# Kernel optimization log

Measured on AMD Instinct MI355X. Metric: run time of the kernel, lower is better.

The kernel has to match this reference:

```python
import jax, jax.numpy as jnp
import numpy as np

H = 32  # num_heads
ROPE_BASE = 10000.0


def _rope(x, offset):
    # x: [B, H, S, D]; rotate-half RoPE with position offset
    B, h, S, D = x.shape
    pos = offset + jnp.arange(S, dtype=jnp.float32)              # [S]
    inv_freq = 1.0 / (ROPE_BASE ** (jnp.arange(0, D, 2, dtype=jnp.float32) / D))  # [D/2]
    ang = pos[:, None] * inv_freq[None, :]                        # [S, D/2]
    cos = jnp.concatenate([jnp.cos(ang), jnp.cos(ang)], axis=-1)  # [S, D]
    sin = jnp.concatenate([jnp.sin(ang), jnp.sin(ang)], axis=-1)  # [S, D]
    x1, x2 = x[..., : D // 2], x[..., D // 2 :]
    rot = jnp.concatenate([-x2, x1], axis=-1)
    return x * cos + rot * sin


def setup_inputs() -> dict:
    key = jax.random.key(0)
    ks = jax.random.split(key, 8)
    B, S, HD = 8, 16, 4096
    Dh = HD // H
    PAST = 4080
    inp = {
        "x": jax.random.normal(ks[0], (B, S, HD), dtype=jnp.float32),
        "past_key": jax.random.normal(ks[1], (B, H, PAST, Dh), dtype=jnp.float32),
        "past_value": jax.random.normal(ks[2], (B, H, PAST, Dh), dtype=jnp.float32),
        "Wq": jax.random.normal(ks[3], (HD, HD), dtype=jnp.float32) * 0.02,
        "bq": jnp.zeros((HD,), dtype=jnp.float32),
        "Wk": jax.random.normal(ks[4], (HD, HD), dtype=jnp.float32) * 0.02,
        "bk": jnp.zeros((HD,), dtype=jnp.float32),
        "Wv": jax.random.normal(ks[5], (HD, HD), dtype=jnp.float32) * 0.02,
        "bv": jnp.zeros((HD,), dtype=jnp.float32),
        "Wo": jax.random.normal(ks[6], (HD, HD), dtype=jnp.float32) * 0.02,
        "bo": jnp.zeros((HD,), dtype=jnp.float32),
    }
    return inp


def reference(x, past_key, past_value, Wq, bq, Wk, bk, Wv, bv, Wo, bo):
    B, S, HD = x.shape
    Dh = HD // H
    scale = Dh ** -0.5
    past_len = past_key.shape[2]

    def split_heads(t):  # [B,S,HD] -> [B,H,S,Dh]
        return t.reshape(B, S, H, Dh).transpose(0, 2, 1, 3)

    Q = split_heads(x @ Wq.T + bq)
    K = split_heads(x @ Wk.T + bk)
    V = split_heads(x @ Wv.T + bv)

    Q = _rope(Q, past_len)
    K = _rope(K, past_len)

    K = jnp.concatenate([past_key, K], axis=2)   # [B,H,past+S,Dh]
    V = jnp.concatenate([past_value, V], axis=2)

    scores = jnp.einsum("bhqd,bhkd->bhqk", Q, K) * scale
    attn = jax.nn.softmax(scores, axis=-1)       # dropout: identity in eval
    out = jnp.einsum("bhqk,bhkd->bhqd", attn, V)
    out = out.transpose(0, 2, 1, 3).reshape(B, S, HD)
    out = out @ Wo.T + bo
    return out, attn, (K, V)
```

## Files before the change

### kernel.cpp

```cpp
#include <hip/hip_runtime.h>
#include <hip/hip_bf16.h>

#define BB 8
#define SS 16
#define HH 32
#define DH 128
#define HD 4096
#define PAST 4080
#define TOT 4096
#define MM 128

#define OUT_O  0
#define ATTN_O 524288
#define K_O    17301504
#define V_O    151519232

#define QR_O 0
#define OH_O 524288
#define RT_O 1048576
#define PW_O 1050624

typedef __attribute__((ext_vector_type(8))) short short8;
typedef __attribute__((ext_vector_type(4))) float f32x4;

static __device__ inline unsigned short f2bf(float x) {
  __hip_bfloat16 h = __float2bfloat16(x);
  return *reinterpret_cast<unsigned short*>(&h);
}

__global__ void rope_table_kernel(float* __restrict__ rt) {
  int t = threadIdx.x;
  int s = t >> 6, j = t & 63;
  double inv = exp(-((double)(2 * j) / 128.0) * log(10000.0));
  double ang = (double)(PAST + s) * inv;
  rt[t] = (float)cos(ang);
  rt[1024 + t] = (float)sin(ang);
}

#define LDP 72
__global__ __launch_bounds__(256) void gemm_mfma(
    const float* __restrict__ A, const float* __restrict__ W0,
    const float* __restrict__ W1, const float* __restrict__ W2,
    float* __restrict__ P) {
  int bx = blockIdx.x;
  int mat = bx >> 8;
  int rem = bx & 255;
  int nc = rem >> 3, ks = rem & 7;
  const float* Wm = (mat == 0) ? W0 : ((mat == 1) ? W1 : W2);
  int n0 = nc * 128;
  int tid = threadIdx.x;
  int lane = tid & 63, wid = tid >> 6;
  int wm = wid >> 1, wn = wid & 1;
  int l15 = lane & 15, l4 = lane >> 4;

  __shared__ unsigned short As[128 * LDP];
  __shared__ unsigned short Bs[128 * LDP];

  f32x4 acc[4][4];
#pragma unroll
  for (int i = 0; i < 4; ++i)
#pragma unroll
    for (int j = 0; j < 4; ++j) acc[i][j] = (f32x4){0.f, 0.f, 0.f, 0.f};

  int srow = tid >> 1;
  int skh = (tid & 1) * 32;

  for (int kt = 0; kt < 8; ++kt) {
    int k0 = ks * 512 + kt * 64;
    const float* Ap = &A[(size_t)srow * 4096 + k0 + skh];
    const float* Wp = &Wm[(size_t)(n0 + srow) * 4096 + k0 + skh];
    float4 va[8], vb[8];
#pragma unroll
    for (int i = 0; i < 8; ++i) {
      va[i] = *(const float4*)(Ap + 4 * i);
      vb[i] = *(const float4*)(Wp + 4 * i);
    }
    __syncthreads();
    unsigned short* Asp = &As[srow * LDP + skh];
    unsigned short* Bsp = &Bs[srow * LDP + skh];
#pragma unroll
    for (int i = 0; i < 8; ++i) {
      ushort4 ua, ub;
      ua.x = f2bf(va[i].x); ua.y = f2bf(va[i].y);
      ua.z = f2bf(va[i].z); ua.w = f2bf(va[i].w);
      ub.x = f2bf(vb[i].x); ub.y = f2bf(vb[i].y);
      ub.z = f2bf(vb[i].z); ub.w = f2bf(vb[i].w);
      *(ushort4*)(Asp + 4 * i) = ua;
      *(ushort4*)(Bsp + 4 * i) = ub;
    }
    __syncthreads();
#pragma unroll
    for (int s = 0; s < 2; ++s) {
      short8 af[4], bf[4];
#pragma unroll
      for (int f = 0; f < 4; ++f) {
        int ar = wm * 64 + f * 16 + l15;
        af[f] = *(const short8*)&As[ar * LDP + s * 32 + l4 * 8];
        int br = wn * 64 + f * 16 + l15;
        bf[f] = *(const short8*)&Bs[br * LDP + s * 32 + l4 * 8];
      }
#pragma unroll
      for (int i = 0; i < 4; ++i)
#pragma unroll
        for (int j = 0; j < 4; ++j)
          acc[i][j] = __builtin_amdgcn_mfma_f32_16x16x32_bf16(
              af[i], bf[j], acc[i][j], 0, 0, 0);
    }
  }

  float* Pb = P + (size_t)(mat * 8 + ks) * 524288 + n0;
#pragma unroll
  for (int i = 0; i < 4; ++i) {
#pragma unroll
    for (int j = 0; j < 4; ++j) {
      int mbase = wm * 64 + i * 16 + l4 * 4;
      int nn = wn * 64 + j * 16 + l15;
#pragma unroll
      for (int r = 0; r < 4; ++r)
        Pb[(size_t)(mbase + r) * 4096 + nn] = acc[i][j][r];
    }
  }
}

__global__ __launch_bounds__(256) void qkv_reduce(
    const float* __restrict__ P, const float* __restrict__ bq,
    const float* __restrict__ bk, const float* __restrict__ bv,
    const float* __restrict__ rt, float* __restrict__ qr,
    float* __restrict__ kout, float* __restrict__ vout) {
  int t = blockIdx.x * 256 + threadIdx.x;
  int d2 = t & 63;
  int h = (t >> 6) & 31;
  int m = (t >> 11) & 127;
  int mat = t >> 18;
  int n1 = h * 128 + d2, n2 = n1 + 64;
  const float* bias = (mat == 0) ? bq : ((mat == 1) ? bk : bv);
  float v1 = bias[n1], v2 = bias[n2];
  const float* Pm = P + (size_t)(mat * 8) * 524288 + (size_t)m * 4096;
#pragma unroll
  for (int s = 0; s < 8; ++s) {
    v1 += Pm[(size_t)s * 524288 + n1];
    v2 += Pm[(size_t)s * 524288 + n2];
  }
  int st = m & 15, b = m >> 4;
  int bh = b * 32 + h;
  if (mat == 2) {
    size_t dst = (size_t)(bh * TOT + PAST + st) * 128;
    vout[dst + d2] = v1; vout[dst + 64 + d2] = v2;
  } else {
    float c = rt[st * 64 + d2], sn = rt[1024 + st * 64 + d2];
    float o1 = v1 * c - v2 * sn;
    float o2 = v2 * c + v1 * sn;
    if (mat == 0) {
      size_t dst = (size_t)(bh * 16 + st) * 128;
      qr[dst + d2] = o1; qr[dst + 64 + d2] = o2;
    } else {
      size_t dst = (size_t)(bh * TOT + PAST + st) * 128;
      kout[dst + d2] = o1; kout[dst + 64 + d2] = o2;
    }
  }
}

__global__ __launch_bounds__(256) void scores_kernel(
    const float* __restrict__ pastk, const float* __restrict__ qr,
    float* __restrict__ kout, float* __restrict__ attn) {
  int bh = blockIdx.x >> 5, kc = blockIdx.x & 31;
  int r0 = kc * 128;
  int tid = threadIdx.x;
  __shared__ float KsT[64][129];
  __shared__ float Qs[2048];
#pragma unroll
  for (int i = 0; i < 8; ++i)
    Qs[tid + i * 256] = qr[(size_t)bh * 2048 + tid + i * 256];

  const float4* pk4 = (const float4*)pastk;
  float4* ko4 = (float4*)kout;
  int qg = tid >> 6, lane = tid & 63;
  float acc[4][2] = {{0.f, 0.f}, {0.f, 0.f}, {0.f, 0.f}, {0.f, 0.f}};

  for (int p = 0; p < 2; ++p) {
    if (p) __syncthreads();
#pragma unroll
    for (int i = 0; i < 8; ++i) {
      int f = tid + i * 256;
      int r = f >> 4, g16 = f & 15;
      int g = g16 + p * 16;
      int row = r0 + r;
      float4 v;
      size_t kidx = (size_t)(bh * TOT + row) * 32 + g;
      if (row < PAST) {
        v = pk4[(size_t)(bh * PAST + row) * 32 + g];
        ko4[kidx] = v;
      } else {
        v = ko4[kidx];
      }
      int dl = g16 * 4;
      KsT[dl][r] = v.x; KsT[dl + 1][r] = v.y;
      KsT[dl + 2][r] = v.z; KsT[dl + 3][r] = v.w;
    }
    __syncthreads();
    int dbase = p * 64;
#pragma unroll 4
    for (int d = 0; d < 64; ++d) {
      float k0v = KsT[d][lane], k1v = KsT[d][lane + 64];
#pragma unroll
      for (int j = 0; j < 4; ++j) {
        float qv = Qs[(qg * 4 + j) * 128 + dbase + d];
        acc[j][0] = fmaf(qv, k0v, acc[j][0]);
        acc[j][1] = fmaf(qv, k1v, acc[j][1]);
      }
    }
  }
  const float scale = 0.088388347648318447f;
#pragma unroll
  for (int j = 0; j < 4; ++j) {
    int q = qg * 4 + j;
    size_t base = (size_t)(bh * 16 + q) * 4096 + r0;
    attn[base + lane] = acc[j][0] * scale;
    attn[base + 64 + lane] = acc[j][1] * scale;
  }
}

__global__ __launch_bounds__(256) void softmax_kernel(float* __restrict__ attn) {
  int row = blockIdx.x;
  float4* a4 = (float4*)(attn + (size_t)row * 4096);
  int tid = threadIdx.x;
  float4 v[4];
  float mx = -1e30f;
#pragma unroll
  for (int i = 0; i < 4; ++i) {
    v[i] = a4[tid + i * 256];
    mx = fmaxf(mx, fmaxf(fmaxf(v[i].x, v[i].y), fmaxf(v[i].z, v[i].w)));
  }
#pragma unroll
  for (int off = 32; off; off >>= 1) mx = fmaxf(mx, __shfl_xor(mx, off));
  __shared__ float redm[4];
  __shared__ float reds[4];
  int wid = tid >> 6;
  if ((tid & 63) == 0) redm[wid] = mx;
  __syncthreads();
  mx = fmaxf(fmaxf(redm[0], redm[1]), fmaxf(redm[2], redm[3]));
  float sum = 0.f;
#pragma unroll
  for (int i = 0; i < 4; ++i) {
    v[i].x = __expf(v[i].x - mx); v[i].y = __expf(v[i].y - mx);
    v[i].z = __expf(v[i].z - mx); v[i].w = __expf(v[i].w - mx);
    sum += v[i].x + v[i].y + v[i].z + v[i].w;
  }
#pragma unroll
  for (int off = 32; off; off >>= 1) sum += __shfl_xor(sum, off);
  if ((tid & 63) == 0) reds[wid] = sum;
  __syncthreads();
  sum = reds[0] + reds[1] + reds[2] + reds[3];
  float inv = 1.f / sum;
#pragma unroll
  for (int i = 0; i < 4; ++i) {
    v[i].x *= inv; v[i].y *= inv; v[i].z *= inv; v[i].w *= inv;
    a4[tid + i * 256] = v[i];
  }
}

__global__ __launch_bounds__(256) void pv_kernel(
    const float* __restrict__ pastv, const float* __restrict__ attn,
    float* __restrict__ vout, float* __restrict__ pvp) {
  int blk = blockIdx.x;
  int bh = blk >> 2, nc = blk & 3;
  int tid = threadIdx.x;
  int dq = tid & 31, rg = tid >> 5;
  __shared__ float atn[16][256];
  __shared__ float red[4][16][128];
  float acc[16][4];
#pragma unroll
  for (int q = 0; q < 16; ++q)
#pragma unroll
    for (int j = 0; j < 4; ++j) acc[q][j] = 0.f;

  const float4* pv4 = (const float4*)pastv;
  float4* vo4 = (float4*)vout;
  int base0 = nc * 1024;

  for (int slab = 0; slab < 4; ++slab) {
    int kbase = base0 + slab * 256;
#pragma unroll
    for (int q = 0; q < 16; ++q)
      atn[q][tid] = attn[(size_t)(bh * 16 + q) * 4096 + kbase + tid];
    __syncthreads();
#pragma unroll 4
    for (int it = 0; it < 32; ++it) {
      int kk = it * 8 + rg;
      int row = kbase + kk;
      float4 v;
      size_t oidx = (size_t)(bh * TOT + row) * 32 + dq;
      if (row < PAST) {
        v = pv4[(size_t)(bh * PAST + row) * 32 + dq];
        vo4[oidx] = v;
      } else {
        v = vo4[oidx];
      }
#pragma unroll
      for (int q = 0; q < 16; ++q) {
        float a = atn[q][kk];
        acc[q][0] = fmaf(a, v.x, acc[q][0]);
        acc[q][1] = fmaf(a, v.y, acc[q][1]);
        acc[q][2] = fmaf(a, v.z, acc[q][2]);
        acc[q][3] = fmaf(a, v.w, acc[q][3]);
      }
    }
    __syncthreads();
  }
#pragma unroll
  for (int q = 0; q < 16; ++q)
#pragma unroll
    for (int j = 0; j < 4; ++j) acc[q][j] += __shfl_xor(acc[q][j], 32);
  int wid = tid >> 6;
  if ((tid & 63) < 32) {
#pragma unroll
    for (int q = 0; q < 16; ++q) {
      float4 o; o.x = acc[q][0]; o.y = acc[q][1]; o.z = acc[q][2]; o.w = acc[q][3];
      *(float4*)&red[wid][q][dq * 4] = o;
    }
  }
  __syncthreads();
#pragma unroll
  for (int rep = 0; rep < 8; ++rep) {
    int o = tid + rep * 256;
    int q = o >> 7, dd = o & 127;
    float s = red[0][q][dd] + red[1][q][dd] + red[2][q][dd] + red[3][q][dd];
    pvp[((size_t)(bh * 4 + nc) * 16 + q) * 128 + dd] = s;
  }
}

__global__ __launch_bounds__(256) void pv_reduce(
    const float* __restrict__ pvp, float* __restrict__ oh) {
  int t = blockIdx.x * 256 + threadIdx.x;
  int dd = t & 127;
  int q = (t >> 7) & 15;
  int bh = t >> 11;
  int b = bh >> 5, h = bh & 31;
  float s = 0.f;
#pragma unroll
  for (int nc = 0; nc < 4; ++nc)
    s += pvp[((size_t)(bh * 4 + nc) * 16 + q) * 128 + dd];
  oh[(size_t)(b * 16 + q) * 4096 + h * 128 + dd] = s;
}

__global__ __launch_bounds__(256) void out_reduce(
    const float* __restrict__ P, const float* __restrict__ bo,
    float* __restrict__ out) {
  int t = blockIdx.x * 256 + threadIdx.x;
  float v = bo[t & 4095];
#pragma unroll
  for (int s = 0; s < 8; ++s) v += P[(size_t)s * 524288 + t];
  out[t] = v;
}

extern "C" void kernel_launch(void* const* d_in, const int* in_sizes, int n_in,
                              void* d_out, int out_size, void* d_ws, size_t ws_size,
                              hipStream_t stream) {
  const float* x     = (const float*)d_in[0];
  const float* pastk = (const float*)d_in[1];
  const float* pastv = (const float*)d_in[2];
  const float* Wq = (const float*)d_in[3];
  const float* bq = (const float*)d_in[4];
  const float* Wk = (const float*)d_in[5];
  const float* bk = (const float*)d_in[6];
  const float* Wv = (const float*)d_in[7];
  const float* bv = (const float*)d_in[8];
  const float* Wo = (const float*)d_in[9];
  const float* bo = (const float*)d_in[10];

  float* out  = (float*)d_out;
  float* attn = out + ATTN_O;
  float* kout = out + K_O;
  float* vout = out + V_O;

  float* ws = (float*)d_ws;
  float* qr = ws + QR_O;
  float* oh = ws + OH_O;
  float* rt = ws + RT_O;
  float* pw = ws + PW_O;

  rope_table_kernel<<<1, 1024, 0, stream>>>(rt);
  gemm_mfma<<<768, 256, 0, stream>>>(x, Wq, Wk, Wv, attn);
  qkv_reduce<<<3072, 256, 0, stream>>>(attn, bq, bk, bv, rt, qr, kout, vout);
  scores_kernel<<<8192, 256, 0, stream>>>(pastk, qr, kout, attn);
  softmax_kernel<<<4096, 256, 0, stream>>>(attn);
  pv_kernel<<<1024, 256, 0, stream>>>(pastv, attn, vout, pw);
  pv_reduce<<<2048, 256, 0, stream>>>(pw, oh);
  gemm_mfma<<<256, 256, 0, stream>>>(oh, Wo, Wo, Wo, pw);
  out_reduce<<<2048, 256, 0, stream>>>(pw, bo, out);
}
```

Before: 739.2 us.

## Fuse softmax into scores and PV kernels via per-chunk online statistics

Drops the standalone softmax pass. The scores kernel now emits a per-128-key-chunk max and exp-sum for each row, a tiny kernel merges these into a row max and inverse sum, and the PV kernel normalizes the attention values while loading them, writing the final probabilities back. This removes one full read and write of the 64 MB attention matrix. It also switches the K/V cache copies to nontemporal loads and stores and unrolls the PV loop by two rows. The stats buffer reuses the workspace region of oh, which is only written later, so that is safe.

```diff
diff --git a/kernel.cpp b/kernel.cpp
--- a/kernel.cpp
+++ b/kernel.cpp
@@ -17,11 +17,14 @@
 
 #define QR_O 0
 #define OH_O 524288
+#define STATS_O 524288
+#define ROWS_O  786432
 #define RT_O 1048576
 #define PW_O 1050624
 
 typedef __attribute__((ext_vector_type(8))) short short8;
 typedef __attribute__((ext_vector_type(4))) float f32x4;
+typedef __attribute__((ext_vector_type(4))) float f4v;
 
 static __device__ inline unsigned short f2bf(float x) {
   __hip_bfloat16 h = __float2bfloat16(x);
@@ -162,7 +165,8 @@
 
 __global__ __launch_bounds__(256) void scores_kernel(
     const float* __restrict__ pastk, const float* __restrict__ qr,
-    float* __restrict__ kout, float* __restrict__ attn) {
+    float* __restrict__ kout, float* __restrict__ attn,
+    float* __restrict__ stats) {
   int bh = blockIdx.x >> 5, kc = blockIdx.x & 31;
   int r0 = kc * 128;
   int tid = threadIdx.x;
@@ -172,8 +176,8 @@
   for (int i = 0; i < 8; ++i)
     Qs[tid + i * 256] = qr[(size_t)bh * 2048 + tid + i * 256];
 
-  const float4* pk4 = (const float4*)pastk;
-  float4* ko4 = (float4*)kout;
+  const f4v* pk4 = (const f4v*)pastk;
+  f4v* ko4 = (f4v*)kout;
   int qg = tid >> 6, lane = tid & 63;
   float acc[4][2] = {{0.f, 0.f}, {0.f, 0.f}, {0.f, 0.f}, {0.f, 0.f}};
 
@@ -185,14 +189,12 @@
       int r = f >> 4, g16 = f & 15;
       int g = g16 + p * 16;
       int row = r0 + r;
-      float4 v;
       size_t kidx = (size_t)(bh * TOT + row) * 32 + g;
-      if (row < PAST) {
-        v = pk4[(size_t)(bh * PAST + row) * 32 + g];
-        ko4[kidx] = v;
-      } else {
-        v = ko4[kidx];
-      }
+      const f4v* src = (row < PAST)
+          ? (pk4 + ((size_t)(bh * PAST + row) * 32 + g))
+          : (const f4v*)(ko4 + kidx);
+      f4v v = __builtin_nontemporal_load(src);
+      if (row < PAST) __builtin_nontemporal_store(v, ko4 + kidx);
       int dl = g16 * 4;
       KsT[dl][r] = v.x; KsT[dl + 1][r] = v.y;
       KsT[dl + 2][r] = v.z; KsT[dl + 3][r] = v.w;
@@ -212,97 +214,111 @@
   }
   const float scale = 0.088388347648318447f;
 #pragma unroll
+  for (int j = 0; j < 4; ++j) { acc[j][0] *= scale; acc[j][1] *= scale; }
+#pragma unroll
   for (int j = 0; j < 4; ++j) {
     int q = qg * 4 + j;
     size_t base = (size_t)(bh * 16 + q) * 4096 + r0;
-    attn[base + lane] = acc[j][0] * scale;
-    attn[base + 64 + lane] = acc[j][1] * scale;
-  }
-}
-
-__global__ __launch_bounds__(256) void softmax_kernel(float* __restrict__ attn) {
-  int row = blockIdx.x;
-  float4* a4 = (float4*)(attn + (size_t)row * 4096);
-  int tid = threadIdx.x;
-  float4 v[4];
-  float mx = -1e30f;
-#pragma unroll
-  for (int i = 0; i < 4; ++i) {
-    v[i] = a4[tid + i * 256];
-    mx = fmaxf(mx, fmaxf(fmaxf(v[i].x, v[i].y), fmaxf(v[i].z, v[i].w)));
-  }
-#pragma unroll
-  for (int off = 32; off; off >>= 1) mx = fmaxf(mx, __shfl_xor(mx, off));
-  __shared__ float redm[4];
-  __shared__ float reds[4];
-  int wid = tid >> 6;
-  if ((tid & 63) == 0) redm[wid] = mx;
-  __syncthreads();
-  mx = fmaxf(fmaxf(redm[0], redm[1]), fmaxf(redm[2], redm[3]));
-  float sum = 0.f;
-#pragma unroll
-  for (int i = 0; i < 4; ++i) {
-    v[i].x = __expf(v[i].x - mx); v[i].y = __expf(v[i].y - mx);
-    v[i].z = __expf(v[i].z - mx); v[i].w = __expf(v[i].w - mx);
-    sum += v[i].x + v[i].y + v[i].z + v[i].w;
-  }
-#pragma unroll
-  for (int off = 32; off; off >>= 1) sum += __shfl_xor(sum, off);
-  if ((tid & 63) == 0) reds[wid] = sum;
-  __syncthreads();
-  sum = reds[0] + reds[1] + reds[2] + reds[3];
-  float inv = 1.f / sum;
-#pragma unroll
-  for (int i = 0; i < 4; ++i) {
-    v[i].x *= inv; v[i].y *= inv; v[i].z *= inv; v[i].w *= inv;
-    a4[tid + i * 256] = v[i];
-  }
+    attn[base + lane] = acc[j][0];
+    attn[base + 64 + lane] = acc[j][1];
+  }
+#pragma unroll
+  for (int j = 0; j < 4; ++j) {
+    float m = fmaxf(acc[j][0], acc[j][1]);
+#pragma unroll
+    for (int off = 32; off; off >>= 1) m = fmaxf(m, __shfl_xor(m, off));
+    float e = __expf(acc[j][0] - m) + __expf(acc[j][1] - m);
+#pragma unroll
+    for (int off = 32; off; off >>= 1) e += __shfl_xor(e, off);
+    if (lane == 0) {
+      int q = qg * 4 + j;
+      size_t si = ((size_t)(bh * 16 + q) * 32 + kc) * 2;
+      stats[si] = m; stats[si + 1] = e;
+    }
+  }
+}
+
+__global__ __launch_bounds__(256) void stats_reduce(
+    const float* __restrict__ stats, float* __restrict__ rows) {
+  int r = blockIdx.x * 256 + threadIdx.x;
+  float m = -1e30f;
+#pragma unroll
+  for (int c = 0; c < 32; ++c) m = fmaxf(m, stats[((size_t)r * 32 + c) * 2]);
+  float s = 0.f;
+#pragma unroll
+  for (int c = 0; c < 32; ++c)
+    s += stats[((size_t)r * 32 + c) * 2 + 1] *
+         __expf(stats[((size_t)r * 32 + c) * 2] - m);
+  rows[r * 2] = m;
+  rows[r * 2 + 1] = 1.f / s;
 }
 
 __global__ __launch_bounds__(256) void pv_kernel(
-    const float* __restrict__ pastv, const float* __restrict__ attn,
-    float* __restrict__ vout, float* __restrict__ pvp) {
+    const float* __restrict__ pastv, float* __restrict__ attn,
+    const float* __restrict__ rows, float* __restrict__ vout,
+    float* __restrict__ pvp) {
   int blk = blockIdx.x;
   int bh = blk >> 2, nc = blk & 3;
   int tid = threadIdx.x;
   int dq = tid & 31, rg = tid >> 5;
   __shared__ float atn[16][256];
   __shared__ float red[4][16][128];
+  __shared__ float sm[16], si[16];
+  if (tid < 16) {
+    sm[tid] = rows[(bh * 16 + tid) * 2];
+    si[tid] = rows[(bh * 16 + tid) * 2 + 1];
+  }
   float acc[16][4];
 #pragma unroll
   for (int q = 0; q < 16; ++q)
 #pragma unroll
     for (int j = 0; j < 4; ++j) acc[q][j] = 0.f;
 
-  const float4* pv4 = (const float4*)pastv;
-  float4* vo4 = (float4*)vout;
+  const f4v* pv4 = (const f4v*)pastv;
+  f4v* vo4 = (f4v*)vout;
   int base0 = nc * 1024;
+  __syncthreads();
 
   for (int slab = 0; slab < 4; ++slab) {
     int kbase = base0 + slab * 256;
 #pragma unroll
-    for (int q = 0; q < 16; ++q)
-      atn[q][tid] = attn[(size_t)(bh * 16 + q) * 4096 + kbase + tid];
+    for (int q = 0; q < 16; ++q) {
+      size_t ai = (size_t)(bh * 16 + q) * 4096 + kbase + tid;
+      float x = attn[ai];
+      float p = __expf(x - sm[q]) * si[q];
+      atn[q][tid] = p;
+      __builtin_nontemporal_store(p, &attn[ai]);
+    }
     __syncthreads();
-#pragma unroll 4
-    for (int it = 0; it < 32; ++it) {
-      int kk = it * 8 + rg;
-      int row = kbase + kk;
-      float4 v;
-      size_t oidx = (size_t)(bh * TOT + row) * 32 + dq;
-      if (row < PAST) {
-        v = pv4[(size_t)(bh * PAST + row) * 32 + dq];
-        vo4[oidx] = v;
-      } else {
-        v = vo4[oidx];
+#pragma unroll 2
+    for (int it = 0; it < 32; it += 2) {
+      int kk0 = it * 8 + rg, kk1 = kk0 + 8;
+      int row0 = kbase + kk0, row1 = kbase + kk1;
+      size_t o0 = (size_t)(bh * TOT + row0) * 32 + dq;
+      size_t o1 = (size_t)(bh * TOT + row1) * 32 + dq;
+      const f4v* s0 = (row0 < PAST)
+          ? (pv4 + ((size_t)(bh * PAST + row0) * 32 + dq)) : (const f4v*)(vo4 + o0);
+      const f4v* s1 = (row1 < PAST)
+          ? (pv4 + ((size_t)(bh * PAST + row1) * 32 + dq)) : (const f4v*)(vo4 + o1);
+      f4v v0 = __builtin_nontemporal_load(s0);
+      f4v v1 = __builtin_nontemporal_load(s1);
+      if (row0 < PAST) __builtin_nontemporal_store(v0, vo4 + o0);
+      if (row1 < PAST) __builtin_nontemporal_store(v1, vo4 + o1);
+#pragma unroll
+      for (int q = 0; q < 16; ++q) {
+        float a = atn[q][kk0];
+        acc[q][0] = fmaf(a, v0.x, acc[q][0]);
+        acc[q][1] = fmaf(a, v0.y, acc[q][1]);
+        acc[q][2] = fmaf(a, v0.z, acc[q][2]);
+        acc[q][3] = fmaf(a, v0.w, acc[q][3]);
       }
 #pragma unroll
       for (int q = 0; q < 16; ++q) {
-        float a = atn[q][kk];
-        acc[q][0] = fmaf(a, v.x, acc[q][0]);
-        acc[q][1] = fmaf(a, v.y, acc[q][1]);
-        acc[q][2] = fmaf(a, v.z, acc[q][2]);
-        acc[q][3] = fmaf(a, v.w, acc[q][3]);
+        float a = atn[q][kk1];
+        acc[q][0] = fmaf(a, v1.x, acc[q][0]);
+        acc[q][1] = fmaf(a, v1.y, acc[q][1]);
+        acc[q][2] = fmaf(a, v1.z, acc[q][2]);
+        acc[q][3] = fmaf(a, v1.w, acc[q][3]);
       }
     }
     __syncthreads();
@@ -315,8 +331,8 @@
   if ((tid & 63) < 32) {
 #pragma unroll
     for (int q = 0; q < 16; ++q) {
-      float4 o; o.x = acc[q][0]; o.y = acc[q][1]; o.z = acc[q][2]; o.w = acc[q][3];
-      *(float4*)&red[wid][q][dq * 4] = o;
+      f4v o; o.x = acc[q][0]; o.y = acc[q][1]; o.z = acc[q][2]; o.w = acc[q][3];
+      *(f4v*)&red[wid][q][dq * 4] = o;
     }
   }
   __syncthreads();
@@ -374,17 +390,19 @@
   float* vout = out + V_O;
 
   float* ws = (float*)d_ws;
-  float* qr = ws + QR_O;
-  float* oh = ws + OH_O;
-  float* rt = ws + RT_O;
-  float* pw = ws + PW_O;
+  float* qr    = ws + QR_O;
+  float* oh    = ws + OH_O;
+  float* stats = ws + STATS_O;
+  float* rows  = ws + ROWS_O;
+  float* rt    = ws + RT_O;
+  float* pw    = ws + PW_O;
 
   rope_table_kernel<<<1, 1024, 0, stream>>>(rt);
   gemm_mfma<<<768, 256, 0, stream>>>(x, Wq, Wk, Wv, attn);
   qkv_reduce<<<3072, 256, 0, stream>>>(attn, bq, bk, bv, rt, qr, kout, vout);
-  scores_kernel<<<8192, 256, 0, stream>>>(pastk, qr, kout, attn);
-  softmax_kernel<<<4096, 256, 0, stream>>>(attn);
-  pv_kernel<<<1024, 256, 0, stream>>>(pastv, attn, vout, pw);
+  scores_kernel<<<8192, 256, 0, stream>>>(pastk, qr, kout, attn, stats);
+  stats_reduce<<<16, 256, 0, stream>>>(stats, rows);
+  pv_kernel<<<1024, 256, 0, stream>>>(pastv, attn, rows, vout, pw);
   pv_reduce<<<2048, 256, 0, stream>>>(pw, oh);
   gemm_mfma<<<256, 256, 0, stream>>>(oh, Wo, Wo, Wo, pw);
   out_reduce<<<2048, 256, 0, stream>>>(pw, bo, out);
```

Result: faster. 643.3 us (-13.0%).
